# Performance work log

Hardware: AMD Instinct MI355X
Metric: run time of the kernel (lower is better)

Reference implementation:

```python
import jax, jax.numpy as jnp
import numpy as np

DIM = 192
HEADS = 6
HIDDEN = 384  # int(dim * mlp_ratio)


def conv2d(x, w, b=None, padding=0, groups=1):
    out = jax.lax.conv_general_dilated(
        x, w, (1, 1), [(padding, padding), (padding, padding)],
        feature_group_count=groups,
        dimension_numbers=('NCHW', 'OIHW', 'NCHW'))
    return out if b is None else out + b[None, :, None, None]


def layernorm(x, g, b, eps=1e-5):
    m = x.mean(-1, keepdims=True)
    v = x.var(-1, keepdims=True)  # biased, matches torch LayerNorm
    return (x - m) / jnp.sqrt(v + eps) * g + b


def l2norm(x, eps=1e-12):  # F.normalize(dim=-1)
    n = jnp.linalg.norm(x, axis=-1, keepdims=True)
    return x / jnp.maximum(n, eps)


def setup_inputs() -> dict:
    key = jax.random.key(0)
    ks = jax.random.split(key, 12)
    s = 0.02
    return {
        'x': jax.random.normal(ks[0], (4, DIM, 128, 128), dtype=jnp.float32),
        'g1': jnp.ones((DIM,), jnp.float32),
        'b1': jnp.zeros((DIM,), jnp.float32),
        'w_qkv': jax.random.normal(ks[1], (3 * DIM, DIM, 1, 1), jnp.float32) * s,
        'w_dw': jax.random.normal(ks[2], (3 * DIM, 1, 3, 3), jnp.float32) * s,
        'temp': jnp.ones((HEADS, 1, 1), jnp.float32),
        'w_head': jax.random.normal(ks[3], (HEADS, HEADS, 3, 3), jnp.float32) * s,
        'w_proj': jax.random.normal(ks[4], (DIM, DIM, 1, 1), jnp.float32) * s,
        'g2': jnp.ones((DIM,), jnp.float32),
        'b2': jnp.zeros((DIM,), jnp.float32),
        'w_fc1': jax.random.normal(ks[5], (HIDDEN, DIM), jnp.float32) * s,
        'b_fc1': jnp.zeros((HIDDEN,), jnp.float32),
        'w_fc2': jax.random.normal(ks[6], (DIM, HIDDEN), jnp.float32) * s,
        'b_fc2': jnp.zeros((DIM,), jnp.float32),
        'w_sa': jax.random.normal(ks[7], (1, DIM, 3, 3), jnp.float32) * s,
        'b_sa': jnp.zeros((1,), jnp.float32),
    }


def reference(x, g1, b1, w_qkv, w_dw, temp, w_head, w_proj, g2, b2,
              w_fc1, b_fc1, w_fc2, b_fc2, w_sa, b_sa):
    b, c, h, w = x.shape
    hw = h * w
    # norm1 (note: original code re-assigns x, so residual uses normed x)
    xf = x.reshape(b, c, hw).transpose(0, 2, 1)          # [b, hw, c]
    x1 = layernorm(xf, g1, b1).transpose(0, 2, 1).reshape(b, c, h, w)
    # channel attention (Restormer style)
    qkv = conv2d(conv2d(x1, w_qkv), w_dw, padding=1, groups=3 * c)
    q, k, v = jnp.split(qkv, 3, axis=1)
    cp = c // HEADS
    q = l2norm(q.reshape(b, HEADS, cp, hw))
    k = l2norm(k.reshape(b, HEADS, cp, hw))
    v = v.reshape(b, HEADS, cp, hw)
    attn = jnp.einsum('bhcn,bhdn->bhcd', q, k) * temp    # [b, heads, cp, cp]
    attn = conv2d(attn, w_head, padding=1)               # conv over head channels
    attn = jax.nn.softmax(attn, axis=-1)
    out = jnp.einsum('bhcd,bhdn->bhcn', attn, v).reshape(b, c, h, w)
    out = conv2d(out, w_proj)
    x2 = x1 + out
    # MLP branch with spatial-gating attn
    x3 = x2.reshape(b, c, hw).transpose(0, 2, 1)         # [b, hw, c]
    y = layernorm(x3, g2, b2)
    y = jax.nn.gelu(y @ w_fc1.T + b_fc1, approximate=False)
    y = y @ w_fc2.T + b_fc2
    y = jax.nn.gelu(y, approximate=False)                # SAAttn act_fn
    y4 = y.reshape(b, h, w, c).transpose(0, 3, 1, 2)     # [b, c, h, w]
    gate = jax.nn.sigmoid(conv2d(y4, w_sa, b_sa, padding=1))  # [b,1,h,w]
    y = (y4 * gate).reshape(b, c, hw).transpose(0, 2, 1)
    x4 = x3 + y
    return x4.transpose(0, 2, 1).reshape(b, c, h, w)
```

## Files before the change

kernel.cpp:

```cpp
#include <hip/hip_runtime.h>
#include <hip/hip_bf16.h>
#include <math.h>

using bf16 = __hip_bfloat16;

static constexpr int CDIM   = 192;
static constexpr int HEADS  = 6;
static constexpr int CP     = 32;
static constexpr int HIDDEN = 384;
static constexpr int HImg   = 128;
static constexpr int WImg   = 128;
static constexpr int HW     = HImg * WImg;
static constexpr int BATCH  = 4;
static constexpr int PCHUNK = 256;
static constexpr int CSPLIT = 12;

typedef __attribute__((ext_vector_type(8))) short short8;
typedef __attribute__((ext_vector_type(4))) float f32x4;
typedef __attribute__((ext_vector_type(4))) unsigned short ushort4v;
typedef __attribute__((ext_vector_type(8))) unsigned short ushort8v;

template<typename T> __device__ inline float tof(T v);
template<> __device__ inline float tof<float>(float v){ return v; }
template<> __device__ inline float tof<bf16>(bf16 v){ return __bfloat162float(v); }

template<typename T> __device__ inline T fromf(float v);
template<> __device__ inline float fromf<float>(float v){ return v; }
template<> __device__ inline bf16  fromf<bf16>(float v){ return __float2bfloat16(v); }

__device__ inline unsigned short f2bf_bits(float f){
    bf16 h = __float2bfloat16(f);
    return *reinterpret_cast<unsigned short*>(&h);
}
__device__ inline float bfbits2f(unsigned short u){
    union { unsigned int i; float f; } c; c.i = ((unsigned int)u) << 16; return c.f;
}

__device__ inline float gelu_exact(float x){
    return 0.5f * x * (1.0f + erff(x * 0.70710678118654752440f));
}

__device__ inline void load4f(const float* p, float* f){
    f32x4 v = *reinterpret_cast<const f32x4*>(p);
    f[0]=v[0]; f[1]=v[1]; f[2]=v[2]; f[3]=v[3];
}
__device__ inline void load4f(const bf16* p, float* f){
    ushort4v v = *reinterpret_cast<const ushort4v*>(p);
    f[0]=bfbits2f(v[0]); f[1]=bfbits2f(v[1]); f[2]=bfbits2f(v[2]); f[3]=bfbits2f(v[3]);
}

__device__ __forceinline__ void gload16(const bf16* g, bf16* l){
    __builtin_amdgcn_global_load_lds(
        (const __attribute__((address_space(1))) void*)g,
        (__attribute__((address_space(3))) void*)l, 16, 0, 0);
}

__global__ __launch_bounds__(256) void convw_kernel(
    const float* __restrict__ w_qkv, const float* __restrict__ w_proj,
    const float* __restrict__ w_fc1, const float* __restrict__ w_fc2,
    bf16* __restrict__ wq, bf16* __restrict__ wp,
    bf16* __restrict__ wf1, bf16* __restrict__ wf2)
{
    int i = blockIdx.x * 256 + threadIdx.x;
    const int n0 = 576*192, n1 = n0 + 192*192, n2 = n1 + 384*192, n3 = n2 + 192*384;
    if (i < n0)      wq[i]       = fromf<bf16>(w_qkv[i]);
    else if (i < n1) wp[i - n0]  = fromf<bf16>(w_proj[i - n0]);
    else if (i < n2) wf1[i - n1] = fromf<bf16>(w_fc1[i - n1]);
    else if (i < n3) wf2[i - n2] = fromf<bf16>(w_fc2[i - n2]);
}

template<typename T, bool WRES>
__global__ __launch_bounds__(256) void ln_fused_kernel(
    const T* __restrict__ in, const float* __restrict__ g,
    const float* __restrict__ b, bf16* __restrict__ resF, bf16* __restrict__ outT)
{
    int z = blockIdx.y, p0 = blockIdx.x * 64;
    __shared__ float tile[CDIM][65];
    __shared__ float sred[4][64], s2red[4][64];
    __shared__ float mrow[64], rrow[64];
    const T* ib = in + (size_t)z * CDIM * HW + p0;
    int tid = threadIdx.x;
    for (int j = tid; j < CDIM * 16; j += 256){
        int c = j >> 4, p4 = (j & 15) * 4;
        float f[4];
        load4f(ib + (size_t)c * HW + p4, f);
        tile[c][p4]   = f[0]; tile[c][p4+1] = f[1];
        tile[c][p4+2] = f[2]; tile[c][p4+3] = f[3];
    }
    __syncthreads();
    int p = tid & 63, q = tid >> 6;
    float s = 0.f, s2 = 0.f;
    #pragma unroll 4
    for (int c = q * 48; c < q * 48 + 48; ++c){
        float v = tile[c][p]; s += v; s2 += v * v;
    }
    sred[q][p] = s; s2red[q][p] = s2;
    __syncthreads();
    if (tid < 64){
        float ts = sred[0][tid] + sred[1][tid] + sred[2][tid] + sred[3][tid];
        float t2 = s2red[0][tid] + s2red[1][tid] + s2red[2][tid] + s2red[3][tid];
        float mean = ts * (1.0f / CDIM);
        float var  = t2 * (1.0f / CDIM) - mean * mean;
        mrow[tid] = mean;
        rrow[tid] = rsqrtf(var + 1e-5f);
    }
    __syncthreads();
    unsigned short* oT = (unsigned short*)(outT + ((size_t)z * HW + p0) * CDIM);
    for (int j = tid; j < 64 * 48; j += 256){
        int pr = j / 48, c4 = (j % 48) * 4;
        float m = mrow[pr], r = rrow[pr];
        ushort4v o;
        #pragma unroll
        for (int k = 0; k < 4; ++k){
            int c = c4 + k;
            o[k] = f2bf_bits((tile[c][pr] - m) * r * g[c] + b[c]);
        }
        *(ushort4v*)&oT[(size_t)pr * CDIM + c4] = o;
    }
    if (WRES){
        unsigned short* oF = (unsigned short*)resF + (size_t)z * CDIM * HW + p0;
        for (int j = tid; j < CDIM * 16; j += 256){
            int c = j >> 4, p4 = (j & 15) * 4;
            float gg = g[c], bb = b[c];
            ushort4v v;
            #pragma unroll
            for (int k = 0; k < 4; ++k)
                v[k] = f2bf_bits((tile[c][p4 + k] - mrow[p4 + k]) * rrow[p4 + k] * gg + bb);
            *(ushort4v*)&oF[(size_t)c * HW + p4] = v;
        }
    }
}

template<int EPI>
__global__ __launch_bounds__(256) void gemm_mfma_kernel(
    const bf16* __restrict__ Wb, const bf16* __restrict__ XT,
    void* __restrict__ Cout, const float* __restrict__ bias,
    const bf16* __restrict__ res, int M, int K)
{
    __shared__ bf16 smem[12288];
    bf16* Als = smem;
    bf16* Bls = smem + 4096;
    int z  = blockIdx.z;
    int n0 = blockIdx.x * 128;
    int m0 = blockIdx.y * 64;
    const bf16* Xb = XT + (size_t)z * (size_t)HW * K;
    int tid  = threadIdx.x;
    int lane = tid & 63, wid = tid >> 6;
    int wm = wid & 1, wn = wid >> 1;
    int r16 = lane & 15, grp = lane >> 4;

    f32x4 acc[2][4];
    #pragma unroll
    for (int i = 0; i < 2; ++i)
        #pragma unroll
        for (int j = 0; j < 4; ++j){ f32x4 zz = {0.f,0.f,0.f,0.f}; acc[i][j] = zz; }

    int nkt = K >> 6;
    for (int kt = 0; kt < nkt; ++kt){
        #pragma unroll
        for (int i = 0; i < 2; ++i){
            int s = i * 256 + tid;
            int row = s >> 3, ch = s & 7;
            gload16(Wb + (size_t)(m0 + row) * K + kt * 64 + ((ch ^ (row & 7)) * 8),
                    Als + s * 8);
        }
        #pragma unroll
        for (int i = 0; i < 4; ++i){
            int s = i * 256 + tid;
            int row = s >> 3, ch = s & 7;
            gload16(Xb + (size_t)(n0 + row) * K + kt * 64 + ((ch ^ (row & 7)) * 8),
                    Bls + s * 8);
        }
        asm volatile("s_waitcnt vmcnt(0)" ::: "memory");
        __syncthreads();
        #pragma unroll
        for (int ks = 0; ks < 2; ++ks){
            int kel = ks * 32 + grp * 8;
            short8 a[2], b[4];
            #pragma unroll
            for (int fi = 0; fi < 2; ++fi){
                int row = wm * 32 + fi * 16 + r16;
                a[fi] = *reinterpret_cast<const short8*>(Als + row * 64 + (kel ^ ((row & 7) * 8)));
            }
            #pragma unroll
            for (int fj = 0; fj < 4; ++fj){
                int row = wn * 64 + fj * 16 + r16;
                b[fj] = *reinterpret_cast<const short8*>(Bls + row * 64 + (kel ^ ((row & 7) * 8)));
            }
            #pragma unroll
            for (int fi = 0; fi < 2; ++fi)
                #pragma unroll
                for (int fj = 0; fj < 4; ++fj)
                    acc[fi][fj] = __builtin_amdgcn_mfma_f32_16x16x32_bf16(
                        a[fi], b[fj], acc[fi][fj], 0, 0, 0);
        }
        __syncthreads();
    }

    if (EPI == 3){
        unsigned short* T = (unsigned short*)smem;
        #pragma unroll
        for (int fi = 0; fi < 2; ++fi)
            #pragma unroll
            for (int fj = 0; fj < 4; ++fj){
                int nl = wn * 64 + fj * 16 + r16;
                int mb = wm * 32 + fi * 16 + grp * 4;
                #pragma unroll
                for (int rr = 0; rr < 4; ++rr){
                    float v = gelu_exact(acc[fi][fj][rr] + bias[m0 + mb + rr]);
                    T[nl * 72 + mb + rr] = f2bf_bits(v);
                }
            }
        __syncthreads();
        bf16* Y = (bf16*)Cout;
        int rrow = tid >> 1, half = tid & 1;
        const short8* srcv = reinterpret_cast<const short8*>(T + rrow * 72 + half * 32);
        short8* dstv = reinterpret_cast<short8*>(
            Y + ((size_t)z * HW + n0 + rrow) * M + m0 + half * 32);
        #pragma unroll
        for (int i = 0; i < 4; ++i) dstv[i] = srcv[i];
        return;
    }

    {
        unsigned short* T = (unsigned short*)smem;
        #pragma unroll
        for (int fi = 0; fi < 2; ++fi)
            #pragma unroll
            for (int fj = 0; fj < 4; ++fj){
                int m = wm * 32 + fi * 16 + grp * 4;
                int n = wn * 64 + fj * 16 + r16;
                #pragma unroll
                for (int rr = 0; rr < 4; ++rr)
                    T[(m + rr) * 136 + n] = f2bf_bits(acc[fi][fj][rr]);
            }
        __syncthreads();
        int row = tid >> 2, c8 = (tid & 3) * 8;
        bf16* Cb = (bf16*)Cout;
        size_t gbase = (size_t)z * M * HW + (size_t)(m0 + row) * HW + n0 + c8;
        float bv = (EPI == 2) ? bias[m0 + row] : 0.f;
        #pragma unroll
        for (int j = 0; j < 4; ++j){
            int coff = j * 32;
            ushort8v t8 = *(const ushort8v*)&T[row * 136 + c8 + coff];
            ushort8v o8;
            if (EPI == 0){
                o8 = t8;
            } else if (EPI == 1){
                ushort8v r8 = *(const ushort8v*)((const unsigned short*)res + gbase + coff);
                #pragma unroll
                for (int k = 0; k < 8; ++k)
                    o8[k] = f2bf_bits(bfbits2f(t8[k]) + bfbits2f(r8[k]));
            } else {
                #pragma unroll
                for (int k = 0; k < 8; ++k)
                    o8[k] = f2bf_bits(gelu_exact(bfbits2f(t8[k]) + bv));
            }
            *(ushort8v*)((unsigned short*)Cb + gbase + coff) = o8;
        }
    }
}

__global__ __launch_bounds__(256) void dw_kernel(
    const bf16* __restrict__ in, const float* __restrict__ wdw,
    bf16* __restrict__ out, float* __restrict__ sqp)
{
    int ch = blockIdx.y, z = blockIdx.z;
    int tid = threadIdx.x;
    int idx = blockIdx.x * 2048 + tid * 8;
    int yy = idx >> 7, xx = idx & 127;
    const unsigned short* p =
        (const unsigned short*)(in + ((size_t)z * 3 * CDIM + ch) * HW);
    float w[9];
    #pragma unroll
    for (int t = 0; t < 9; ++t) w[t] = wdw[ch * 9 + t];
    float f[3][8], lf[3], rf[3];
    #pragma unroll
    for (int dy = 0; dy < 3; ++dy){
        int iy = yy + dy - 1;
        if (iy >= 0 && iy < HImg){
            ushort8v v8 = *(const ushort8v*)(p + iy * WImg + xx);
            #pragma unroll
            for (int j = 0; j < 8; ++j) f[dy][j] = bfbits2f(v8[j]);
        } else {
            #pragma unroll
            for (int j = 0; j < 8; ++j) f[dy][j] = 0.f;
        }
        float l = __shfl_up(f[dy][7], 1);
        float r = __shfl_down(f[dy][0], 1);
        lf[dy] = (xx == 0) ? 0.f : l;
        rf[dy] = (xx + 8 >= WImg) ? 0.f : r;
    }
    ushort8v o8;
    float sq = 0.f;
    #pragma unroll
    for (int j = 0; j < 8; ++j){
        float a = 0.f;
        #pragma unroll
        for (int dy = 0; dy < 3; ++dy){
            float e0 = (j == 0) ? lf[dy] : f[dy][j - 1];
            float e2 = (j == 7) ? rf[dy] : f[dy][j + 1];
            a = fmaf(w[dy*3], e0, fmaf(w[dy*3+1], f[dy][j], fmaf(w[dy*3+2], e2, a)));
        }
        o8[j] = f2bf_bits(a);
        sq = fmaf(a, a, sq);
    }
    *(ushort8v*)((unsigned short*)(out + ((size_t)z * 3 * CDIM + ch) * HW) + idx) = o8;
    if (ch < 2 * CDIM){
        #pragma unroll
        for (int m = 1; m < 64; m <<= 1) sq += __shfl_xor(sq, m, 64);
        __shared__ float red[4];
        if ((tid & 63) == 0) red[tid >> 6] = sq;
        __syncthreads();
        if (tid == 0)
            sqp[((size_t)ch * BATCH + z) * 8 + blockIdx.x] =
                red[0] + red[1] + red[2] + red[3];
    }
}

__global__ __launch_bounds__(256) void attn_qk_kernel(
    const bf16* __restrict__ qkv, const float* __restrict__ sqp,
    const float* __restrict__ temp, float* __restrict__ part)
{
    int chunk = blockIdx.x;
    int h = blockIdx.y, z = blockIdx.z;
    __shared__ unsigned short qs[CP][PCHUNK + 4];
    __shared__ unsigned short ks[CP][PCHUNK + 4];
    __shared__ float invqs[CP], invks[CP];
    int tid = threadIdx.x;
    if (tid < 2 * CP){
        int which = tid >> 5, cc = tid & 31;
        int ch = which * CDIM + h * CP + cc;
        const float* sp = &sqp[((size_t)ch * BATCH + z) * 8];
        float s = sp[0]+sp[1]+sp[2]+sp[3]+sp[4]+sp[5]+sp[6]+sp[7];
        float inv = 1.0f / fmaxf(sqrtf(s), 1e-12f);
        (which ? invks : invqs)[cc] = inv;
    }
    int n0 = chunk * PCHUNK;
    const unsigned short* qb = (const unsigned short*)(qkv + ((size_t)z * 3 * CDIM + h * CP) * HW);
    const unsigned short* kb = (const unsigned short*)(qkv + ((size_t)z * 3 * CDIM + CDIM + h * CP) * HW);
    for (int i = tid; i < CP * (PCHUNK / 4); i += 256){
        int r = i >> 6, p4 = i & 63;
        *(ushort4v*)&qs[r][p4 * 4] = *(const ushort4v*)&qb[(size_t)r * HW + n0 + p4 * 4];
        *(ushort4v*)&ks[r][p4 * 4] = *(const ushort4v*)&kb[(size_t)r * HW + n0 + p4 * 4];
    }
    __syncthreads();
    int c  = tid >> 3;
    int d0 = (tid & 7) * 4;
    float acc[4] = {0.f, 0.f, 0.f, 0.f};
    for (int p4 = 0; p4 < PCHUNK / 4; ++p4){
        ushort4v qv = *(const ushort4v*)&qs[c][p4 * 4];
        float qf0 = bfbits2f(qv[0]), qf1 = bfbits2f(qv[1]);
        float qf2 = bfbits2f(qv[2]), qf3 = bfbits2f(qv[3]);
        #pragma unroll
        for (int j = 0; j < 4; ++j){
            ushort4v kv = *(const ushort4v*)&ks[d0 + j][p4 * 4];
            acc[j] = fmaf(qf0, bfbits2f(kv[0]),
                     fmaf(qf1, bfbits2f(kv[1]),
                     fmaf(qf2, bfbits2f(kv[2]),
                     fmaf(qf3, bfbits2f(kv[3]), acc[j]))));
        }
    }
    float sc = invqs[c] * temp[h];
    size_t base = ((size_t)chunk * BATCH * HEADS + (size_t)z * HEADS + h) * CP * CP
                + c * CP + d0;
    #pragma unroll
    for (int j = 0; j < 4; ++j)
        part[base + j] = acc[j] * sc * invks[d0 + j];
}

__global__ __launch_bounds__(256) void attn_reduce_kernel(
    const float* __restrict__ part, float* __restrict__ attn)
{
    int idx = blockIdx.x * 256 + threadIdx.x;
    float s = 0.f;
    for (int ch = 0; ch < HW / PCHUNK; ++ch)
        s += part[(size_t)ch * (BATCH * HEADS * CP * CP) + idx];
    attn[idx] = s;
}

__global__ __launch_bounds__(256) void headconv_softmax_kernel(
    const float* __restrict__ attn, const float* __restrict__ wh,
    float* __restrict__ attn2)
{
    int oh = blockIdx.x, z = blockIdx.y;
    __shared__ float wsm[HEADS * 9];
    __shared__ float ain[HEADS][CP * CP];
    __shared__ float aout[CP * CP];
    int tid = threadIdx.x;
    if (tid < HEADS * 9) wsm[tid] = wh[oh * HEADS * 9 + tid];
    for (int i = tid; i < HEADS * CP * CP; i += 256)
        ain[i >> 10][i & 1023] = attn[((size_t)z * HEADS + (i >> 10)) * CP * CP + (i & 1023)];
    __syncthreads();
    for (int idx = tid; idx < CP * CP; idx += 256){
        int i = idx >> 5, j = idx & 31;
        float acc = 0.f;
        #pragma unroll
        for (int ih = 0; ih < HEADS; ++ih){
            #pragma unroll
            for (int dy = 0; dy < 3; ++dy){
                int ii = i + dy - 1;
                if (ii < 0 || ii >= CP) continue;
                #pragma unroll
                for (int dx = 0; dx < 3; ++dx){
                    int jj = j + dx - 1;
                    if (jj < 0 || jj >= CP) continue;
                    acc += wsm[ih * 9 + dy * 3 + dx] * ain[ih][ii * CP + jj];
                }
            }
        }
        aout[idx] = acc;
    }
    __syncthreads();
    int r = tid >> 3, l8 = tid & 7;
    float v[4];
    #pragma unroll
    for (int k = 0; k < 4; ++k) v[k] = aout[r * CP + l8 * 4 + k];
    float mx = fmaxf(fmaxf(v[0], v[1]), fmaxf(v[2], v[3]));
    #pragma unroll
    for (int m = 1; m < 8; m <<= 1) mx = fmaxf(mx, __shfl_xor(mx, m, 64));
    float sum = 0.f;
    #pragma unroll
    for (int k = 0; k < 4; ++k){ v[k] = expf(v[k] - mx); sum += v[k]; }
    #pragma unroll
    for (int m = 1; m < 8; m <<= 1) sum += __shfl_xor(sum, m, 64);
    float rs = 1.0f / sum;
    float* o = attn2 + ((size_t)z * HEADS + oh) * CP * CP + r * CP + l8 * 4;
    #pragma unroll
    for (int k = 0; k < 4; ++k) o[k] = v[k] * rs;
}

__global__ __launch_bounds__(256) void av_kernel(
    const float* __restrict__ attn2, const bf16* __restrict__ qkv, bf16* __restrict__ outT)
{
    int h = blockIdx.y, z = blockIdx.z;
    int tid = threadIdx.x;
    __shared__ float As[CP][CP];
    __shared__ unsigned short Vs[CP][PCHUNK];
    __shared__ unsigned short ot[256][36];
    for (int i = tid; i < CP * CP; i += 256)
        As[i >> 5][i & 31] = attn2[((size_t)(z * HEADS + h)) * CP * CP + i];
    int n0 = blockIdx.x * 256;
    const unsigned short* vb =
        (const unsigned short*)(qkv + ((size_t)z * 3 * CDIM + 2 * CDIM + h * CP) * HW) + n0;
    for (int i = tid; i < CP * 64; i += 256){
        int d = i >> 6, p4 = (i & 63) * 4;
        *(ushort4v*)&Vs[d][p4] = *(const ushort4v*)(vb + (size_t)d * HW + p4);
    }
    __syncthreads();
    float vreg[CP];
    #pragma unroll
    for (int d = 0; d < CP; ++d) vreg[d] = bfbits2f(Vs[d][tid]);
    for (int c = 0; c < CP; ++c){
        float acc = 0.f;
        #pragma unroll
        for (int d = 0; d < CP; ++d) acc = fmaf(As[c][d], vreg[d], acc);
        ot[tid][c] = f2bf_bits(acc);
    }
    __syncthreads();
    unsigned short* ob = (unsigned short*)outT
        + ((size_t)z * HW + (size_t)n0) * CDIM + h * CP;
    for (int j = tid; j < 256 * 8; j += 256){
        int row = j >> 3, q4 = (j & 7) * 4;
        *(ushort4v*)&ob[(size_t)row * CDIM + q4] = *(ushort4v*)&ot[row][q4];
    }
}

__global__ __launch_bounds__(256) void gate_partial_kernel(
    const bf16* __restrict__ y, const float* __restrict__ wsa,
    float* __restrict__ part_g)
{
    int cs = blockIdx.y, z = blockIdx.z;
    __shared__ float wsm[16 * 9];
    if (threadIdx.x < 144) wsm[threadIdx.x] = wsa[cs * 144 + threadIdx.x];
    __syncthreads();
    int idx = blockIdx.x * 2048 + threadIdx.x * 8;
    int yy = idx >> 7, xx = idx & 127;
    const unsigned short* yb =
        (const unsigned short*)(y + (size_t)z * CDIM * HW + (size_t)cs * 16 * HW);
    float acc[8] = {0.f,0.f,0.f,0.f,0.f,0.f,0.f,0.f};
    for (int c = 0; c < 16; ++c){
        const unsigned short* pc = yb + (size_t)c * HW;
        #pragma unroll
        for (int dy = 0; dy < 3; ++dy){
            int iy = yy + dy - 1;
            float f[8], lf, rf;
            if (iy >= 0 && iy < HImg){
                ushort8v v8 = *(const ushort8v*)(pc + iy * WImg + xx);
                #pragma unroll
                for (int j = 0; j < 8; ++j) f[j] = bfbits2f(v8[j]);
            } else {
                #pragma unroll
                for (int j = 0; j < 8; ++j) f[j] = 0.f;
            }
            float l = __shfl_up(f[7], 1);
            float r = __shfl_down(f[0], 1);
            lf = (xx == 0) ? 0.f : l;
            rf = (xx + 8 >= WImg) ? 0.f : r;
            const float* wr = &wsm[c * 9 + dy * 3];
            #pragma unroll
            for (int j = 0; j < 8; ++j){
                float e0 = (j == 0) ? lf : f[j - 1];
                float e2 = (j == 7) ? rf : f[j + 1];
                acc[j] = fmaf(wr[0], e0, fmaf(wr[1], f[j], fmaf(wr[2], e2, acc[j])));
            }
        }
    }
    float* og = &part_g[((size_t)cs * BATCH + z) * HW + idx];
    f32x4 o0 = {acc[0], acc[1], acc[2], acc[3]};
    f32x4 o1 = {acc[4], acc[5], acc[6], acc[7]};
    *(f32x4*)og = o0;
    *(f32x4*)(og + 4) = o1;
}

__global__ __launch_bounds__(256) void gate_finish_kernel(
    const float* __restrict__ part_g, const float* __restrict__ bsa,
    float* __restrict__ gate)
{
    int i4 = (blockIdx.x * 256 + threadIdx.x) * 4;
    float b0 = bsa[0];
    f32x4 acc = {b0, b0, b0, b0};
    #pragma unroll
    for (int cs = 0; cs < CSPLIT; ++cs){
        f32x4 v = *(const f32x4*)&part_g[(size_t)cs * BATCH * HW + i4];
        #pragma unroll
        for (int j = 0; j < 4; ++j) acc[j] += v[j];
    }
    f32x4 o;
    #pragma unroll
    for (int j = 0; j < 4; ++j) o[j] = 1.0f / (1.0f + expf(-acc[j]));
    *(f32x4*)&gate[i4] = o;
}

__global__ __launch_bounds__(256) void final_kernel(
    const bf16* __restrict__ x2, const bf16* __restrict__ y2,
    const float* __restrict__ gate, float* __restrict__ out)
{
    size_t i8 = ((size_t)blockIdx.x * 256 + threadIdx.x) * 8;
    int n = (int)(i8 % HW);
    int z = (int)(i8 / ((size_t)CDIM * HW));
    ushort8v a8 = *(const ushort8v*)((const unsigned short*)x2 + i8);
    ushort8v b8 = *(const ushort8v*)((const unsigned short*)y2 + i8);
    const float* gp = gate + (size_t)z * HW + n;
    f32x4 g0 = *(const f32x4*)gp;
    f32x4 g1 = *(const f32x4*)(gp + 4);
    f32x4 o0, o1;
    #pragma unroll
    for (int j = 0; j < 4; ++j){
        o0[j] = bfbits2f(a8[j])     + bfbits2f(b8[j])     * g0[j];
        o1[j] = bfbits2f(a8[j + 4]) + bfbits2f(b8[j + 4]) * g1[j];
    }
    *(f32x4*)(out + i8) = o0;
    *(f32x4*)(out + i8 + 4) = o1;
}

extern "C" void kernel_launch(void* const* d_in, const int* in_sizes, int n_in,
                              void* d_out, int out_size, void* d_ws, size_t ws_size,
                              hipStream_t stream)
{
    const float* x      = (const float*)d_in[0];
    const float* g1     = (const float*)d_in[1];
    const float* b1     = (const float*)d_in[2];
    const float* w_qkv  = (const float*)d_in[3];
    const float* w_dw   = (const float*)d_in[4];
    const float* temp   = (const float*)d_in[5];
    const float* w_head = (const float*)d_in[6];
    const float* w_proj = (const float*)d_in[7];
    const float* g2     = (const float*)d_in[8];
    const float* b2     = (const float*)d_in[9];
    const float* w_fc1  = (const float*)d_in[10];
    const float* b_fc1  = (const float*)d_in[11];
    const float* w_fc2  = (const float*)d_in[12];
    const float* b_fc2  = (const float*)d_in[13];
    const float* w_sa   = (const float*)d_in[14];
    const float* b_sa   = (const float*)d_in[15];
    float* out = (float*)d_out;

    char* ws = (char*)d_ws;
    const size_t FULL = (size_t)BATCH * CDIM * HW;

    bf16* x1 = (bf16*)ws;
    bf16* y2 = x1;
    char* R1 = ws + FULL * 2;
    bf16*  qkvA      = (bf16*)R1;
    bf16*  attn_outT = (bf16*)R1;
    bf16*  ln2T      = (bf16*)R1;
    bf16*  y1T       = (bf16*)(R1 + FULL * 2);
    char* R2 = R1 + FULL * 3 * 2;
    bf16*  x1T = (bf16*)R2;
    bf16*  dwB = (bf16*)R2;
    bf16*  x2  = (bf16*)R2;
    char* SM = R2 + FULL * 3 * 2;
    float* attn   = (float*)SM;
    float* attn2  = attn + BATCH * HEADS * CP * CP;
    float* gate   = attn2 + BATCH * HEADS * CP * CP;
    float* sqp    = gate + BATCH * HW;
    float* part   = sqp + 2 * CDIM * BATCH * 8;
    float* part_g = part;
    bf16* wq_b  = (bf16*)(part + (HW / PCHUNK) * BATCH * HEADS * CP * CP);
    bf16* wp_b  = wq_b  + 576 * 192;
    bf16* wf1_b = wp_b  + 192 * 192;
    bf16* wf2_b = wf1_b + 384 * 192;

    dim3 blk(256);

    convw_kernel<<<dim3((294912 + 255) / 256), blk, 0, stream>>>(
        w_qkv, w_proj, w_fc1, w_fc2, wq_b, wp_b, wf1_b, wf2_b);
    ln_fused_kernel<float, true><<<dim3(HW / 64, BATCH), blk, 0, stream>>>(
        x, g1, b1, x1, x1T);
    gemm_mfma_kernel<0><<<dim3(HW / 128, (3 * CDIM) / 64, BATCH), blk, 0, stream>>>(
        wq_b, x1T, qkvA, nullptr, nullptr, 3 * CDIM, CDIM);
    dw_kernel<<<dim3(HW / 2048, 3 * CDIM, BATCH), blk, 0, stream>>>(qkvA, w_dw, dwB, sqp);
    attn_qk_kernel<<<dim3(HW / PCHUNK, HEADS, BATCH), blk, 0, stream>>>(
        dwB, sqp, temp, part);
    attn_reduce_kernel<<<dim3((BATCH * HEADS * CP * CP) / 256), blk, 0, stream>>>(part, attn);
    headconv_softmax_kernel<<<dim3(HEADS, BATCH), blk, 0, stream>>>(attn, w_head, attn2);
    av_kernel<<<dim3(HW / 256, HEADS, BATCH), blk, 0, stream>>>(attn2, dwB, attn_outT);
    gemm_mfma_kernel<1><<<dim3(HW / 128, CDIM / 64, BATCH), blk, 0, stream>>>(
        wp_b, attn_outT, x2, nullptr, x1, CDIM, CDIM);
    ln_fused_kernel<bf16, false><<<dim3(HW / 64, BATCH), blk, 0, stream>>>(
        x2, g2, b2, nullptr, ln2T);
    gemm_mfma_kernel<3><<<dim3(HW / 128, HIDDEN / 64, BATCH), blk, 0, stream>>>(
        wf1_b, ln2T, y1T, b_fc1, nullptr, HIDDEN, CDIM);
    gemm_mfma_kernel<2><<<dim3(HW / 128, CDIM / 64, BATCH), blk, 0, stream>>>(
        wf2_b, y1T, y2, b_fc2, nullptr, CDIM, HIDDEN);
    gate_partial_kernel<<<dim3(HW / 2048, CSPLIT, BATCH), blk, 0, stream>>>(
        y2, w_sa, part_g);
    gate_finish_kernel<<<dim3(BATCH * HW / 1024), blk, 0, stream>>>(part_g, b_sa, gate);
    final_kernel<<<dim3((int)(FULL / 2048)), blk, 0, stream>>>(x2, y2, gate, out);
}
```

Measured before the change: 290.0 us.

## Double-buffer GEMM LDS tiles and compute two rows per thread in depthwise conv

The MFMA GEMM now prefetches the next K tile into a second LDS buffer while computing the current one, waiting only on the older loads. The depthwise 3x3 kernel has each thread produce two output rows from four loaded input rows, which cuts redundant input reads and halves the grid. Doubled shared memory per block may lower occupancy, and the partial norm sums now use 4 chunks instead of 8.

```diff
diff --git a/kernel.cpp b/kernel.cpp
--- a/kernel.cpp
+++ b/kernel.cpp
@@ -14,6 +14,7 @@
 static constexpr int BATCH  = 4;
 static constexpr int PCHUNK = 256;
 static constexpr int CSPLIT = 12;
+static constexpr int DWCHUNK = 4;
 
 typedef __attribute__((ext_vector_type(8))) short short8;
 typedef __attribute__((ext_vector_type(4))) float f32x4;
@@ -137,9 +138,7 @@
     void* __restrict__ Cout, const float* __restrict__ bias,
     const bf16* __restrict__ res, int M, int K)
 {
-    __shared__ bf16 smem[12288];
-    bf16* Als = smem;
-    bf16* Bls = smem + 4096;
+    __shared__ bf16 smem[24576];
     int z  = blockIdx.z;
     int n0 = blockIdx.x * 128;
     int m0 = blockIdx.y * 64;
@@ -155,24 +154,38 @@
         #pragma unroll
         for (int j = 0; j < 4; ++j){ f32x4 zz = {0.f,0.f,0.f,0.f}; acc[i][j] = zz; }
 
-    int nkt = K >> 6;
-    for (int kt = 0; kt < nkt; ++kt){
+    auto STAGE = [&](int kt, int buf){
+        bf16* Al = smem + buf * 12288;
+        bf16* Bl = Al + 4096;
         #pragma unroll
         for (int i = 0; i < 2; ++i){
             int s = i * 256 + tid;
             int row = s >> 3, ch = s & 7;
             gload16(Wb + (size_t)(m0 + row) * K + kt * 64 + ((ch ^ (row & 7)) * 8),
-                    Als + s * 8);
+                    Al + s * 8);
         }
         #pragma unroll
         for (int i = 0; i < 4; ++i){
             int s = i * 256 + tid;
             int row = s >> 3, ch = s & 7;
             gload16(Xb + (size_t)(n0 + row) * K + kt * 64 + ((ch ^ (row & 7)) * 8),
-                    Bls + s * 8);
-        }
-        asm volatile("s_waitcnt vmcnt(0)" ::: "memory");
-        __syncthreads();
+                    Bl + s * 8);
+        }
+    };
+
+    int nkt = K >> 6;
+    STAGE(0, 0);
+    int cur = 0;
+    for (int kt = 0; kt < nkt; ++kt){
+        if (kt + 1 < nkt){
+            STAGE(kt + 1, cur ^ 1);
+            asm volatile("s_waitcnt vmcnt(6)" ::: "memory");
+        } else {
+            asm volatile("s_waitcnt vmcnt(0)" ::: "memory");
+        }
+        __builtin_amdgcn_s_barrier();
+        bf16* Al = smem + cur * 12288;
+        bf16* Bl = Al + 4096;
         #pragma unroll
         for (int ks = 0; ks < 2; ++ks){
             int kel = ks * 32 + grp * 8;
@@ -180,12 +193,12 @@
             #pragma unroll
             for (int fi = 0; fi < 2; ++fi){
                 int row = wm * 32 + fi * 16 + r16;
-                a[fi] = *reinterpret_cast<const short8*>(Als + row * 64 + (kel ^ ((row & 7) * 8)));
+                a[fi] = *reinterpret_cast<const short8*>(Al + row * 64 + (kel ^ ((row & 7) * 8)));
             }
             #pragma unroll
             for (int fj = 0; fj < 4; ++fj){
                 int row = wn * 64 + fj * 16 + r16;
-                b[fj] = *reinterpret_cast<const short8*>(Bls + row * 64 + (kel ^ ((row & 7) * 8)));
+                b[fj] = *reinterpret_cast<const short8*>(Bl + row * 64 + (kel ^ ((row & 7) * 8)));
             }
             #pragma unroll
             for (int fi = 0; fi < 2; ++fi)
@@ -194,7 +207,10 @@
                     acc[fi][fj] = __builtin_amdgcn_mfma_f32_16x16x32_bf16(
                         a[fi], b[fj], acc[fi][fj], 0, 0, 0);
         }
-        __syncthreads();
+        asm volatile("s_waitcnt lgkmcnt(0)" ::: "memory");
+        __builtin_amdgcn_sched_barrier(0);
+        __builtin_amdgcn_s_barrier();
+        cur ^= 1;
     }
 
     if (EPI == 3){
@@ -267,45 +283,51 @@
 {
     int ch = blockIdx.y, z = blockIdx.z;
     int tid = threadIdx.x;
-    int idx = blockIdx.x * 2048 + tid * 8;
-    int yy = idx >> 7, xx = idx & 127;
+    int rp = tid >> 4;
+    int xx = (tid & 15) * 8;
+    int y0 = blockIdx.x * 32 + rp * 2;
     const unsigned short* p =
         (const unsigned short*)(in + ((size_t)z * 3 * CDIM + ch) * HW);
     float w[9];
     #pragma unroll
     for (int t = 0; t < 9; ++t) w[t] = wdw[ch * 9 + t];
-    float f[3][8], lf[3], rf[3];
-    #pragma unroll
-    for (int dy = 0; dy < 3; ++dy){
-        int iy = yy + dy - 1;
+    float f[4][8], lf[4], rf[4];
+    #pragma unroll
+    for (int r = 0; r < 4; ++r){
+        int iy = y0 - 1 + r;
         if (iy >= 0 && iy < HImg){
             ushort8v v8 = *(const ushort8v*)(p + iy * WImg + xx);
             #pragma unroll
-            for (int j = 0; j < 8; ++j) f[dy][j] = bfbits2f(v8[j]);
+            for (int j = 0; j < 8; ++j) f[r][j] = bfbits2f(v8[j]);
         } else {
             #pragma unroll
-            for (int j = 0; j < 8; ++j) f[dy][j] = 0.f;
-        }
-        float l = __shfl_up(f[dy][7], 1);
-        float r = __shfl_down(f[dy][0], 1);
-        lf[dy] = (xx == 0) ? 0.f : l;
-        rf[dy] = (xx + 8 >= WImg) ? 0.f : r;
-    }
-    ushort8v o8;
+            for (int j = 0; j < 8; ++j) f[r][j] = 0.f;
+        }
+        float l = __shfl_up(f[r][7], 1);
+        float rr_ = __shfl_down(f[r][0], 1);
+        lf[r] = (xx == 0) ? 0.f : l;
+        rf[r] = (xx + 8 >= WImg) ? 0.f : rr_;
+    }
     float sq = 0.f;
-    #pragma unroll
-    for (int j = 0; j < 8; ++j){
-        float a = 0.f;
-        #pragma unroll
-        for (int dy = 0; dy < 3; ++dy){
-            float e0 = (j == 0) ? lf[dy] : f[dy][j - 1];
-            float e2 = (j == 7) ? rf[dy] : f[dy][j + 1];
-            a = fmaf(w[dy*3], e0, fmaf(w[dy*3+1], f[dy][j], fmaf(w[dy*3+2], e2, a)));
-        }
-        o8[j] = f2bf_bits(a);
-        sq = fmaf(a, a, sq);
-    }
-    *(ushort8v*)((unsigned short*)(out + ((size_t)z * 3 * CDIM + ch) * HW) + idx) = o8;
+    unsigned short* ob = (unsigned short*)(out + ((size_t)z * 3 * CDIM + ch) * HW);
+    #pragma unroll
+    for (int orow = 0; orow < 2; ++orow){
+        ushort8v o8;
+        #pragma unroll
+        for (int j = 0; j < 8; ++j){
+            float a = 0.f;
+            #pragma unroll
+            for (int dy = 0; dy < 3; ++dy){
+                int r = orow + dy;
+                float e0 = (j == 0) ? lf[r] : f[r][j - 1];
+                float e2 = (j == 7) ? rf[r] : f[r][j + 1];
+                a = fmaf(w[dy*3], e0, fmaf(w[dy*3+1], f[r][j], fmaf(w[dy*3+2], e2, a)));
+            }
+            o8[j] = f2bf_bits(a);
+            sq = fmaf(a, a, sq);
+        }
+        *(ushort8v*)(ob + (y0 + orow) * WImg + xx) = o8;
+    }
     if (ch < 2 * CDIM){
         #pragma unroll
         for (int m = 1; m < 64; m <<= 1) sq += __shfl_xor(sq, m, 64);
@@ -313,7 +335,7 @@
         if ((tid & 63) == 0) red[tid >> 6] = sq;
         __syncthreads();
         if (tid == 0)
-            sqp[((size_t)ch * BATCH + z) * 8 + blockIdx.x] =
+            sqp[((size_t)ch * BATCH + z) * DWCHUNK + blockIdx.x] =
                 red[0] + red[1] + red[2] + red[3];
     }
 }
@@ -331,8 +353,8 @@
     if (tid < 2 * CP){
         int which = tid >> 5, cc = tid & 31;
         int ch = which * CDIM + h * CP + cc;
-        const float* sp = &sqp[((size_t)ch * BATCH + z) * 8];
-        float s = sp[0]+sp[1]+sp[2]+sp[3]+sp[4]+sp[5]+sp[6]+sp[7];
+        const float* sp = &sqp[((size_t)ch * BATCH + z) * DWCHUNK];
+        float s = sp[0] + sp[1] + sp[2] + sp[3];
         float inv = 1.0f / fmaxf(sqrtf(s), 1e-12f);
         (which ? invks : invqs)[cc] = inv;
     }
@@ -595,7 +617,7 @@
     float* attn2  = attn + BATCH * HEADS * CP * CP;
     float* gate   = attn2 + BATCH * HEADS * CP * CP;
     float* sqp    = gate + BATCH * HW;
-    float* part   = sqp + 2 * CDIM * BATCH * 8;
+    float* part   = sqp + 2 * CDIM * BATCH * DWCHUNK;
     float* part_g = part;
     bf16* wq_b  = (bf16*)(part + (HW / PCHUNK) * BATCH * HEADS * CP * CP);
     bf16* wp_b  = wq_b  + 576 * 192;
@@ -610,7 +632,7 @@
         x, g1, b1, x1, x1T);
     gemm_mfma_kernel<0><<<dim3(HW / 128, (3 * CDIM) / 64, BATCH), blk, 0, stream>>>(
         wq_b, x1T, qkvA, nullptr, nullptr, 3 * CDIM, CDIM);
-    dw_kernel<<<dim3(HW / 2048, 3 * CDIM, BATCH), blk, 0, stream>>>(qkvA, w_dw, dwB, sqp);
+    dw_kernel<<<dim3(DWCHUNK, 3 * CDIM, BATCH), blk, 0, stream>>>(qkvA, w_dw, dwB, sqp);
     attn_qk_kernel<<<dim3(HW / PCHUNK, HEADS, BATCH), blk, 0, stream>>>(
         dwB, sqp, temp, part);
     attn_reduce_kernel<<<dim3((BATCH * HEADS * CP * CP) / 256), blk, 0, stream>>>(part, attn);
```

New measurement: 289.5 us. About the same (-0.2%).
